# Kernel optimization log

Hardware: AMD Instinct MI355X
Metric: run time of the kernel (lower is better)

## Reference

```python
import jax, jax.numpy as jnp
import numpy as np

B, N, C, H = 8, 4096, 384, 8
HD = C // H  # 48
KERNEL_EPS = 1e-3
EPS = 1e-8


def setup_inputs() -> dict:
    key = jax.random.key(0)
    k1, k2, k3, k4 = jax.random.split(key, 4)
    x = jax.random.normal(k1, (B, N, C), dtype=jnp.float32)
    Wqkv = jax.random.normal(k2, (3 * C, C), dtype=jnp.float32) * 0.02
    Wproj = jax.random.normal(k3, (C, C), dtype=jnp.float32) * 0.02
    bproj = jax.random.normal(k4, (C,), dtype=jnp.float32) * 0.02
    return {"x": x, "Wqkv": Wqkv, "Wproj": Wproj, "bproj": bproj}


def reference(x, Wqkv, Wproj, bproj):
    # qkv projection (no bias): (B,N,3C) -> (3,B,H,N,HD)
    qkv = jnp.einsum('bnc,dc->bnd', x, Wqkv).reshape(B, N, 3, H, HD)
    qkv = jnp.transpose(qkv, (2, 0, 3, 1, 4))
    q, k, v = qkv[0], qkv[1], qkv[2]

    # generalized_kernel with projection_matrix=None, kernel_fn=ReLU
    dn = HD ** (-0.25)  # data normalizer
    qp = jax.nn.relu(dn * q) + KERNEL_EPS  # (B,H,N,HD) feature map, m=HD
    kp = jax.nn.relu(dn * k) + KERNEL_EPS

    ks = kp.sum(axis=2)                              # (B,H,m)
    D = jnp.einsum('bhnm,bhm->bhn', qp, ks)          # (B,H,N)
    kptv = jnp.einsum('bhnd,bhnm->bhdm', v, kp)      # (B,H,HD,m)
    out = jnp.einsum('bhnm,bhdm->bhnd', qp, kptv) / (D[..., None] + EPS)

    # faithful to original: reshape (B,H,N,HD) -> (B,N,C) WITHOUT head transpose
    out = out.reshape(B, N, C)
    return jnp.einsum('bnc,dc->bnd', out, Wproj) + bproj
```

## Files before the change

kernel.cpp:

```cpp
#include <hip/hip_runtime.h>
#include <hip/hip_bf16.h>


typedef __attribute__((ext_vector_type(8))) short short8;
typedef __attribute__((ext_vector_type(4))) float floatx4;

#define MFMA(a, b, c) __builtin_amdgcn_mfma_f32_16x16x32_bf16((a), (b), (c), 0, 0, 0)

__device__ __forceinline__ unsigned short f2bf(float f) {
  union { float f; unsigned u; } x; x.f = f;
  unsigned r = x.u + 0x7FFFu + ((x.u >> 16) & 1u);
  return (unsigned short)(r >> 16);
}

__device__ __forceinline__ void cv4(const float* __restrict__ in, unsigned short* __restrict__ out, int i) {
  float4 v = *(const float4*)(in + i);
  uint2 o;
  o.x = (unsigned)f2bf(v.x) | ((unsigned)f2bf(v.y) << 16);
  o.y = (unsigned)f2bf(v.z) | ((unsigned)f2bf(v.w) << 16);
  *(uint2*)(out + i) = o;
}

__global__ void conv_all(const float* __restrict__ x, const float* __restrict__ wq,
                         const float* __restrict__ wp,
                         unsigned short* __restrict__ xb, unsigned short* __restrict__ wqb,
                         unsigned short* __restrict__ wpb, float* __restrict__ accD) {
  const int tid = blockIdx.x * blockDim.x + threadIdx.x;
  const int stride = gridDim.x * blockDim.x * 4;
  for (int i = tid * 4; i < 12582912; i += stride) cv4(x, xb, i);
  for (int i = tid * 4; i < 442368; i += stride) cv4(wq, wqb, i);
  for (int i = tid * 4; i < 147456; i += stride) cv4(wp, wpb, i);
  float4 z = {0.f, 0.f, 0.f, 0.f};
  for (int i = tid * 4; i < 196608; i += stride) *(float4*)(accD + i) = z;
}

template <int EPI>
__global__ __launch_bounds__(256, 3) void gemm_bt(
    const unsigned short* __restrict__ A,
    const unsigned short* __restrict__ Bt,
    void* __restrict__ Cout,
    unsigned short* __restrict__ Kt,
    unsigned short* __restrict__ Vt,
    const float* __restrict__ bias,
    int M, int N, int K, int ldc) {
  __shared__ unsigned short As[128 * 64];
  __shared__ unsigned short Bs[128 * 64];
  const int NT = N >> 7;
  const int cpx = gridDim.x >> 3;
  const int bid = (blockIdx.x & 7) * cpx + (blockIdx.x >> 3);
  const int bn = bid % NT;
  const int bm = bid / NT;
  const int tid = threadIdx.x;
  const int w = tid >> 6, lane = tid & 63;
  const int wm = w >> 1, wn = w & 1;
  const int l15 = lane & 15, l4 = lane >> 4;

  floatx4 zero = {0.f, 0.f, 0.f, 0.f};
  floatx4 acc[4][4];
#pragma unroll
  for (int i = 0; i < 4; ++i)
#pragma unroll
    for (int j = 0; j < 4; ++j) acc[i][j] = zero;

  const int li0 = (w * 4) * 64 + lane;
  const size_t Abase = (size_t)(bm * 128) * K;
  const size_t Bbase = (size_t)(bn * 128) * K;

  for (int k0 = 0; k0 < K; k0 += 64) {
#pragma unroll
    for (int i = 0; i < 4; ++i) {
      int li = li0 + i * 64;
      int row = li >> 3;
      int col = (li & 7) << 3;
      const unsigned short* gA = A + Abase + (size_t)row * K + k0 + col;
      const unsigned short* gB = Bt + Bbase + (size_t)row * K + k0 + col;
      __builtin_amdgcn_global_load_lds((const __attribute__((address_space(1))) void*)gA,
                                       (__attribute__((address_space(3))) void*)&As[(w * 4 + i) * 512],
                                       16, 0, 0);
      __builtin_amdgcn_global_load_lds((const __attribute__((address_space(1))) void*)gB,
                                       (__attribute__((address_space(3))) void*)&Bs[(w * 4 + i) * 512],
                                       16, 0, 0);
    }
    __syncthreads();
#pragma unroll
    for (int kk = 0; kk < 2; ++kk) {
      short8 a[4], b[4];
#pragma unroll
      for (int mf = 0; mf < 4; ++mf)
        a[mf] = *(const short8*)&As[(wm * 64 + mf * 16 + l15) * 64 + kk * 32 + l4 * 8];
#pragma unroll
      for (int nf = 0; nf < 4; ++nf)
        b[nf] = *(const short8*)&Bs[(wn * 64 + nf * 16 + l15) * 64 + kk * 32 + l4 * 8];
#pragma unroll
      for (int mf = 0; mf < 4; ++mf)
#pragma unroll
        for (int nf = 0; nf < 4; ++nf)
          acc[mf][nf] = MFMA(a[mf], b[nf], acc[mf][nf]);
    }
    __syncthreads();
  }

  const float DN = 0.3799178430f;
  if (EPI == 1) {
#pragma unroll
    for (int mf = 0; mf < 4; ++mf) {
#pragma unroll
      for (int nf = 0; nf < 4; ++nf) {
        int gm0 = bm * 128 + wm * 64 + mf * 16 + l4 * 4;
        int gn = bn * 128 + wn * 64 + nf * 16 + l15;
#pragma unroll
        for (int r = 0; r < 4; ++r)
          ((float*)Cout)[(size_t)(gm0 + r) * ldc + gn] = acc[mf][nf][r] + bias[gn];
      }
    }
  } else if (bn < 3) {
#pragma unroll
    for (int mf = 0; mf < 4; ++mf) {
#pragma unroll
      for (int nf = 0; nf < 4; ++nf) {
        int gm0 = bm * 128 + wm * 64 + mf * 16 + l4 * 4;
        int gn = bn * 128 + wn * 64 + nf * 16 + l15;
#pragma unroll
        for (int r = 0; r < 4; ++r) {
          float v = fmaxf(acc[mf][nf][r] * DN, 0.f) + 1e-3f;
          ((unsigned short*)Cout)[(size_t)(gm0 + r) * 384 + gn] = f2bf(v);
        }
      }
    }
  } else {
    const int isV = (bn >= 6);
    unsigned short* T = isV ? Vt : Kt;
    const int fbase = bn * 128 - (isV ? 768 : 384) + wn * 64;
    const int b = (bm * 128) >> 12;
    const int tokb = ((bm * 128) & 4095) + wm * 64;
#pragma unroll
    for (int nf = 0; nf < 4; ++nf) {
      int fk = fbase + nf * 16 + l15;
      int h = fk / 48;
      int m = fk - h * 48;
      unsigned short* dst = T + (((size_t)(b * 8 + h) * 48 + m) << 12);
#pragma unroll
      for (int mf = 0; mf < 4; ++mf) {
        int tok = tokb + mf * 16 + l4 * 4;
        float v0 = acc[mf][nf][0], v1 = acc[mf][nf][1];
        float v2 = acc[mf][nf][2], v3 = acc[mf][nf][3];
        if (!isV) {
          v0 = fmaxf(v0 * DN, 0.f) + 1e-3f;
          v1 = fmaxf(v1 * DN, 0.f) + 1e-3f;
          v2 = fmaxf(v2 * DN, 0.f) + 1e-3f;
          v3 = fmaxf(v3 * DN, 0.f) + 1e-3f;
        }
        uint2 o;
        o.x = (unsigned)f2bf(v0) | ((unsigned)f2bf(v1) << 16);
        o.y = (unsigned)f2bf(v2) | ((unsigned)f2bf(v3) << 16);
        *(uint2*)(dst + tok) = o;
      }
    }
  }
}

__global__ __launch_bounds__(256, 4) void attn_ksum(
    const unsigned short* __restrict__ Kt,
    const unsigned short* __restrict__ Vt,
    float* __restrict__ accD) {
  const int bh = blockIdx.x >> 3, g = blockIdx.x & 7;
  const int tid = threadIdx.x, w = tid >> 6, lane = tid & 63;
  const int l15 = lane & 15, l4 = lane >> 4;
  __shared__ float red[64 * 48];

  floatx4 zero = {0.f, 0.f, 0.f, 0.f};
  floatx4 acc[4][3];
#pragma unroll
  for (int i = 0; i < 4; ++i)
#pragma unroll
    for (int j = 0; j < 3; ++j) acc[i][j] = zero;

  unsigned short ov = (l15 == 0) ? (unsigned short)0x3F80 : (unsigned short)0;
  short8 ones;
#pragma unroll
  for (int e = 0; e < 8; ++e) ones[e] = (short)ov;

  const size_t base = (size_t)bh * 48 * 4096;
  const int tok0 = g * 512 + w * 128 + l4 * 8;

#pragma unroll
  for (int c = 0; c < 4; ++c) {
    int t0 = tok0 + c * 32;
    short8 a[3], bb[3];
#pragma unroll
    for (int f = 0; f < 3; ++f) {
      a[f] = *(const short8*)&Vt[base + (size_t)(f * 16 + l15) * 4096 + t0];
      bb[f] = *(const short8*)&Kt[base + (size_t)(f * 16 + l15) * 4096 + t0];
    }
#pragma unroll
    for (int af = 0; af < 3; ++af)
#pragma unroll
      for (int bf = 0; bf < 3; ++bf)
        acc[af][bf] = MFMA(a[af], bb[bf], acc[af][bf]);
#pragma unroll
    for (int bf = 0; bf < 3; ++bf)
      acc[3][bf] = MFMA(ones, bb[bf], acc[3][bf]);
  }

  for (int i = tid; i < 64 * 48; i += 256) red[i] = 0.f;
  __syncthreads();
#pragma unroll
  for (int af = 0; af < 4; ++af)
#pragma unroll
    for (int bf = 0; bf < 3; ++bf)
#pragma unroll
      for (int r = 0; r < 4; ++r)
        atomicAdd(&red[(af * 16 + l4 * 4 + r) * 48 + bf * 16 + l15], acc[af][bf][r]);
  __syncthreads();
  float* dst = accD + (size_t)bh * 64 * 48;
  for (int i = tid; i < 64 * 48; i += 256) atomicAdd(&dst[i], red[i]);
}

__global__ __launch_bounds__(256, 2) void attn_out(
    const unsigned short* __restrict__ qp,
    const float* __restrict__ accD,
    unsigned short* __restrict__ outr) {
  const int bh = blockIdx.x >> 4, tg = blockIdx.x & 15;
  const int b = bh >> 3, h = bh & 7;
  const int tid = threadIdx.x, w = tid >> 6, lane = tid & 63;
  const int l15 = lane & 15, l4 = lane >> 4;
  const int t0 = tg * 256 + w * 64;

  short8 bfr[2][4];
#pragma unroll
  for (int kk = 0; kk < 2; ++kk) {
#pragma unroll
    for (int nf = 0; nf < 4; ++nf) {
      int row = nf * 16 + l15;
      int c0 = kk * 32 + l4 * 8;
      short8 f;
      if (kk == 1 && l4 >= 2) {
#pragma unroll
        for (int e = 0; e < 8; ++e) f[e] = 0;
      } else {
        const float* p = accD + (size_t)bh * 3072 + row * 48 + c0;
        float4 v0 = *(const float4*)p;
        float4 v1 = *(const float4*)(p + 4);
        f[0] = (short)f2bf(v0.x); f[1] = (short)f2bf(v0.y);
        f[2] = (short)f2bf(v0.z); f[3] = (short)f2bf(v0.w);
        f[4] = (short)f2bf(v1.x); f[5] = (short)f2bf(v1.y);
        f[6] = (short)f2bf(v1.z); f[7] = (short)f2bf(v1.w);
      }
      bfr[kk][nf] = f;
    }
  }

  floatx4 zero = {0.f, 0.f, 0.f, 0.f};
  floatx4 acc[4][4];
#pragma unroll
  for (int i = 0; i < 4; ++i)
#pragma unroll
    for (int j = 0; j < 4; ++j) acc[i][j] = zero;

  const size_t rb = (size_t)b * 4096;
#pragma unroll
  for (int mf = 0; mf < 4; ++mf) {
#pragma unroll
    for (int kk = 0; kk < 2; ++kk) {
      int tt = t0 + mf * 16 + l15;
      short8 a = *(const short8*)&qp[(rb + tt) * 384 + h * 48 + kk * 32 + l4 * 8];
#pragma unroll
      for (int nf = 0; nf < 4; ++nf)
        acc[mf][nf] = MFMA(a, bfr[kk][nf], acc[mf][nf]);
    }
  }

#pragma unroll
  for (int mf = 0; mf < 4; ++mf) {
    float den[4];
#pragma unroll
    for (int r = 0; r < 4; ++r)
      den[r] = __shfl(acc[mf][3][r], lane & 48, 64) + 1e-8f;
#pragma unroll
    for (int nf = 0; nf < 3; ++nf) {
#pragma unroll
      for (int r = 0; r < 4; ++r) {
        int tt = t0 + mf * 16 + l4 * 4 + r;
        int d = nf * 16 + l15;
        float v = acc[mf][nf][r] / den[r];
        int np = h * 512 + (tt >> 3);
        int cp = (tt & 7) * 48 + d;
        outr[(rb + np) * 384 + cp] = f2bf(v);
      }
    }
  }
}

extern "C" void kernel_launch(void* const* d_in, const int* in_sizes, int n_in,
                              void* d_out, int out_size, void* d_ws, size_t ws_size,
                              hipStream_t stream) {
  const float* x = (const float*)d_in[0];
  const float* Wqkv = (const float*)d_in[1];
  const float* Wproj = (const float*)d_in[2];
  const float* bproj = (const float*)d_in[3];

  char* ws = (char*)d_ws;
  unsigned short* xb = (unsigned short*)(ws);
  unsigned short* wqkvb = (unsigned short*)(ws + 25165824);
  unsigned short* wprojb = (unsigned short*)(ws + 26050560);
  unsigned short* qp = (unsigned short*)(ws + 26345472);
  unsigned short* Kt = (unsigned short*)(ws + 51511552);
  unsigned short* Vt = (unsigned short*)(ws + 76677376);
  float* accD = (float*)(ws + 101843200);
  unsigned short* outr = (unsigned short*)(ws + 102629632);

  conv_all<<<2048, 256, 0, stream>>>(x, Wqkv, Wproj, xb, wqkvb, wprojb, accD);
  gemm_bt<0><<<2304, 256, 0, stream>>>(xb, wqkvb, (void*)qp, Kt, Vt, nullptr, 32768, 1152, 384, 384);
  attn_ksum<<<512, 256, 0, stream>>>(Kt, Vt, accD);
  attn_out<<<1024, 256, 0, stream>>>(qp, accD, outr);
  gemm_bt<1><<<768, 256, 0, stream>>>(outr, wprojb, d_out, nullptr, nullptr, bproj, 32768, 384, 384, 384);
}
```

Before: 224.0 us.

## Fuse x conversion and K^T V reduction into the QKV GEMM

The QKV GEMM now reads fp32 x directly and converts it to bf16 while staging into shared memory, which removes the separate full-size x conversion pass. K and V tiles for each head are kept in shared memory and reduced immediately into the K^T V and K-sum accumulators with MFMA and global atomics. This drops the Kt/Vt intermediate buffers and the attn_ksum kernel. In exchange the GEMM loads A with non-async vector loads, uses more shared memory (fewer blocks per CU), launches more blocks, and issues many more global atomics.

```diff
diff --git a/kernel.cpp b/kernel.cpp
--- a/kernel.cpp
+++ b/kernel.cpp
@@ -21,199 +21,169 @@
   *(uint2*)(out + i) = o;
 }
 
-__global__ void conv_all(const float* __restrict__ x, const float* __restrict__ wq,
-                         const float* __restrict__ wp,
-                         unsigned short* __restrict__ xb, unsigned short* __restrict__ wqb,
-                         unsigned short* __restrict__ wpb, float* __restrict__ accD) {
+__global__ void conv_w(const float* __restrict__ wq, const float* __restrict__ wp,
+                       unsigned short* __restrict__ wqb, unsigned short* __restrict__ wpb,
+                       float* __restrict__ accD) {
   const int tid = blockIdx.x * blockDim.x + threadIdx.x;
   const int stride = gridDim.x * blockDim.x * 4;
-  for (int i = tid * 4; i < 12582912; i += stride) cv4(x, xb, i);
   for (int i = tid * 4; i < 442368; i += stride) cv4(wq, wqb, i);
   for (int i = tid * 4; i < 147456; i += stride) cv4(wp, wpb, i);
   float4 z = {0.f, 0.f, 0.f, 0.f};
   for (int i = tid * 4; i < 196608; i += stride) *(float4*)(accD + i) = z;
 }
 
-template <int EPI>
-__global__ __launch_bounds__(256, 3) void gemm_bt(
-    const unsigned short* __restrict__ A,
-    const unsigned short* __restrict__ Bt,
-    void* __restrict__ Cout,
-    unsigned short* __restrict__ Kt,
-    unsigned short* __restrict__ Vt,
-    const float* __restrict__ bias,
-    int M, int N, int K, int ldc) {
+__global__ __launch_bounds__(256, 2) void gemm_qkv(
+    const float* __restrict__ x,
+    const unsigned short* __restrict__ Wq,
+    unsigned short* __restrict__ qp,
+    float* __restrict__ accD) {
   __shared__ unsigned short As[128 * 64];
   __shared__ unsigned short Bs[128 * 64];
-  const int NT = N >> 7;
+  __shared__ unsigned short Tt[2][48 * 136];
+
   const int cpx = gridDim.x >> 3;
   const int bid = (blockIdx.x & 7) * cpx + (blockIdx.x >> 3);
-  const int bn = bid % NT;
-  const int bm = bid / NT;
+  const int mt = bid / 11;
+  const int j = bid - mt * 11;
   const int tid = threadIdx.x;
   const int w = tid >> 6, lane = tid & 63;
   const int wm = w >> 1, wn = w & 1;
   const int l15 = lane & 15, l4 = lane >> 4;
+  const int isQ = (j < 3);
+  const int h = j - 3;
 
   floatx4 zero = {0.f, 0.f, 0.f, 0.f};
   floatx4 acc[4][4];
 #pragma unroll
   for (int i = 0; i < 4; ++i)
 #pragma unroll
-    for (int j = 0; j < 4; ++j) acc[i][j] = zero;
-
-  const int li0 = (w * 4) * 64 + lane;
-  const size_t Abase = (size_t)(bm * 128) * K;
-  const size_t Bbase = (size_t)(bn * 128) * K;
-
-  for (int k0 = 0; k0 < K; k0 += 64) {
-#pragma unroll
-    for (int i = 0; i < 4; ++i) {
-      int li = li0 + i * 64;
-      int row = li >> 3;
-      int col = (li & 7) << 3;
-      const unsigned short* gA = A + Abase + (size_t)row * K + k0 + col;
-      const unsigned short* gB = Bt + Bbase + (size_t)row * K + k0 + col;
-      __builtin_amdgcn_global_load_lds((const __attribute__((address_space(1))) void*)gA,
-                                       (__attribute__((address_space(3))) void*)&As[(w * 4 + i) * 512],
-                                       16, 0, 0);
-      __builtin_amdgcn_global_load_lds((const __attribute__((address_space(1))) void*)gB,
-                                       (__attribute__((address_space(3))) void*)&Bs[(w * 4 + i) * 512],
-                                       16, 0, 0);
+    for (int jj = 0; jj < 4; ++jj) acc[i][jj] = zero;
+
+  const size_t Abase = (size_t)mt * 128 * 384;
+  const int arow = tid >> 4;
+  const int akf = (tid & 15) * 4;
+
+  for (int k0 = 0; k0 < 384; k0 += 64) {
+#pragma unroll
+    for (int p = 0; p < 8; ++p) {
+      int row = p * 16 + arow;
+      float4 v = *(const float4*)&x[Abase + (size_t)row * 384 + k0 + akf];
+      uint2 o;
+      o.x = (unsigned)f2bf(v.x) | ((unsigned)f2bf(v.y) << 16);
+      o.y = (unsigned)f2bf(v.z) | ((unsigned)f2bf(v.w) << 16);
+      *(uint2*)&As[row * 64 + akf] = o;
+    }
+    if (isQ) {
+      const size_t Bb = (size_t)(j * 128) * 384;
+#pragma unroll
+      for (int i = 0; i < 4; ++i) {
+        int li = w * 256 + i * 64 + lane;
+        int row = li >> 3, col = (li & 7) << 3;
+        __builtin_amdgcn_global_load_lds(
+            (const __attribute__((address_space(1))) void*)(Wq + Bb + (size_t)row * 384 + k0 + col),
+            (__attribute__((address_space(3))) void*)&Bs[row * 64 + col], 16, 0, 0);
+      }
+    } else {
+#pragma unroll
+      for (int i = 0; i < 3; ++i) {
+        int idx = i * 256 + tid;
+        int row = idx >> 3, col = (idx & 7) << 3;
+        int srow = (row < 48) ? (384 + h * 48 + row) : (720 + h * 48 + row);
+        __builtin_amdgcn_global_load_lds(
+            (const __attribute__((address_space(1))) void*)(Wq + (size_t)srow * 384 + k0 + col),
+            (__attribute__((address_space(3))) void*)&Bs[row * 64 + col], 16, 0, 0);
+      }
     }
     __syncthreads();
 #pragma unroll
     for (int kk = 0; kk < 2; ++kk) {
-      short8 a[4], b[4];
+      short8 a[4];
 #pragma unroll
       for (int mf = 0; mf < 4; ++mf)
         a[mf] = *(const short8*)&As[(wm * 64 + mf * 16 + l15) * 64 + kk * 32 + l4 * 8];
-#pragma unroll
-      for (int nf = 0; nf < 4; ++nf)
-        b[nf] = *(const short8*)&Bs[(wn * 64 + nf * 16 + l15) * 64 + kk * 32 + l4 * 8];
-#pragma unroll
-      for (int mf = 0; mf < 4; ++mf)
-#pragma unroll
-        for (int nf = 0; nf < 4; ++nf)
-          acc[mf][nf] = MFMA(a[mf], b[nf], acc[mf][nf]);
+      if (isQ) {
+#pragma unroll
+        for (int nf = 0; nf < 4; ++nf) {
+          short8 b = *(const short8*)&Bs[(wn * 64 + nf * 16 + l15) * 64 + kk * 32 + l4 * 8];
+#pragma unroll
+          for (int mf = 0; mf < 4; ++mf) acc[mf][nf] = MFMA(a[mf], b, acc[mf][nf]);
+        }
+      } else {
+#pragma unroll
+        for (int nf = 0; nf < 3; ++nf) {
+          short8 b = *(const short8*)&Bs[(wn * 48 + nf * 16 + l15) * 64 + kk * 32 + l4 * 8];
+#pragma unroll
+          for (int mf = 0; mf < 4; ++mf) acc[mf][nf] = MFMA(a[mf], b, acc[mf][nf]);
+        }
+      }
     }
     __syncthreads();
   }
 
   const float DN = 0.3799178430f;
-  if (EPI == 1) {
+  if (isQ) {
 #pragma unroll
     for (int mf = 0; mf < 4; ++mf) {
 #pragma unroll
       for (int nf = 0; nf < 4; ++nf) {
-        int gm0 = bm * 128 + wm * 64 + mf * 16 + l4 * 4;
-        int gn = bn * 128 + wn * 64 + nf * 16 + l15;
-#pragma unroll
-        for (int r = 0; r < 4; ++r)
-          ((float*)Cout)[(size_t)(gm0 + r) * ldc + gn] = acc[mf][nf][r] + bias[gn];
-      }
-    }
-  } else if (bn < 3) {
-#pragma unroll
-    for (int mf = 0; mf < 4; ++mf) {
-#pragma unroll
-      for (int nf = 0; nf < 4; ++nf) {
-        int gm0 = bm * 128 + wm * 64 + mf * 16 + l4 * 4;
-        int gn = bn * 128 + wn * 64 + nf * 16 + l15;
+        int gm0 = mt * 128 + wm * 64 + mf * 16 + l4 * 4;
+        int gn = j * 128 + wn * 64 + nf * 16 + l15;
 #pragma unroll
         for (int r = 0; r < 4; ++r) {
           float v = fmaxf(acc[mf][nf][r] * DN, 0.f) + 1e-3f;
-          ((unsigned short*)Cout)[(size_t)(gm0 + r) * 384 + gn] = f2bf(v);
+          qp[(size_t)(gm0 + r) * 384 + gn] = f2bf(v);
         }
       }
     }
   } else {
-    const int isV = (bn >= 6);
-    unsigned short* T = isV ? Vt : Kt;
-    const int fbase = bn * 128 - (isV ? 768 : 384) + wn * 64;
-    const int b = (bm * 128) >> 12;
-    const int tokb = ((bm * 128) & 4095) + wm * 64;
-#pragma unroll
-    for (int nf = 0; nf < 4; ++nf) {
-      int fk = fbase + nf * 16 + l15;
-      int h = fk / 48;
-      int m = fk - h * 48;
-      unsigned short* dst = T + (((size_t)(b * 8 + h) * 48 + m) << 12);
+#pragma unroll
+    for (int nf = 0; nf < 3; ++nf) {
 #pragma unroll
       for (int mf = 0; mf < 4; ++mf) {
-        int tok = tokb + mf * 16 + l4 * 4;
-        float v0 = acc[mf][nf][0], v1 = acc[mf][nf][1];
-        float v2 = acc[mf][nf][2], v3 = acc[mf][nf][3];
-        if (!isV) {
-          v0 = fmaxf(v0 * DN, 0.f) + 1e-3f;
-          v1 = fmaxf(v1 * DN, 0.f) + 1e-3f;
-          v2 = fmaxf(v2 * DN, 0.f) + 1e-3f;
-          v3 = fmaxf(v3 * DN, 0.f) + 1e-3f;
+#pragma unroll
+        for (int r = 0; r < 4; ++r) {
+          float v = acc[mf][nf][r];
+          if (wn == 0) v = fmaxf(v * DN, 0.f) + 1e-3f;
+          Tt[wn][(nf * 16 + l15) * 136 + wm * 64 + mf * 16 + l4 * 4 + r] = f2bf(v);
         }
-        uint2 o;
-        o.x = (unsigned)f2bf(v0) | ((unsigned)f2bf(v1) << 16);
-        o.y = (unsigned)f2bf(v2) | ((unsigned)f2bf(v3) << 16);
-        *(uint2*)(dst + tok) = o;
-      }
-    }
-  }
-}
-
-__global__ __launch_bounds__(256, 4) void attn_ksum(
-    const unsigned short* __restrict__ Kt,
-    const unsigned short* __restrict__ Vt,
-    float* __restrict__ accD) {
-  const int bh = blockIdx.x >> 3, g = blockIdx.x & 7;
-  const int tid = threadIdx.x, w = tid >> 6, lane = tid & 63;
-  const int l15 = lane & 15, l4 = lane >> 4;
-  __shared__ float red[64 * 48];
-
-  floatx4 zero = {0.f, 0.f, 0.f, 0.f};
-  floatx4 acc[4][3];
-#pragma unroll
-  for (int i = 0; i < 4; ++i)
-#pragma unroll
-    for (int j = 0; j < 3; ++j) acc[i][j] = zero;
-
-  unsigned short ov = (l15 == 0) ? (unsigned short)0x3F80 : (unsigned short)0;
-  short8 ones;
-#pragma unroll
-  for (int e = 0; e < 8; ++e) ones[e] = (short)ov;
-
-  const size_t base = (size_t)bh * 48 * 4096;
-  const int tok0 = g * 512 + w * 128 + l4 * 8;
-
-#pragma unroll
-  for (int c = 0; c < 4; ++c) {
-    int t0 = tok0 + c * 32;
-    short8 a[3], bb[3];
-#pragma unroll
-    for (int f = 0; f < 3; ++f) {
-      a[f] = *(const short8*)&Vt[base + (size_t)(f * 16 + l15) * 4096 + t0];
-      bb[f] = *(const short8*)&Kt[base + (size_t)(f * 16 + l15) * 4096 + t0];
-    }
-#pragma unroll
-    for (int af = 0; af < 3; ++af)
-#pragma unroll
-      for (int bf = 0; bf < 3; ++bf)
-        acc[af][bf] = MFMA(a[af], bb[bf], acc[af][bf]);
-#pragma unroll
-    for (int bf = 0; bf < 3; ++bf)
-      acc[3][bf] = MFMA(ones, bb[bf], acc[3][bf]);
-  }
-
-  for (int i = tid; i < 64 * 48; i += 256) red[i] = 0.f;
-  __syncthreads();
-#pragma unroll
-  for (int af = 0; af < 4; ++af)
-#pragma unroll
-    for (int bf = 0; bf < 3; ++bf)
-#pragma unroll
-      for (int r = 0; r < 4; ++r)
-        atomicAdd(&red[(af * 16 + l4 * 4 + r) * 48 + bf * 16 + l15], acc[af][bf][r]);
-  __syncthreads();
-  float* dst = accD + (size_t)bh * 64 * 48;
-  for (int i = tid; i < 64 * 48; i += 256) atomicAdd(&dst[i], red[i]);
+      }
+    }
+    __syncthreads();
+    short8 ones;
+    {
+      unsigned short ov = (l15 == 0) ? (unsigned short)0x3F80 : (unsigned short)0;
+#pragma unroll
+      for (int e = 0; e < 8; ++e) ones[e] = (short)ov;
+    }
+    floatx4 acc2[3];
+#pragma unroll
+    for (int i = 0; i < 3; ++i) acc2[i] = zero;
+#pragma unroll
+    for (int c = 0; c < 4; ++c) {
+      short8 af;
+      if (w < 3)
+        af = *(const short8*)&Tt[1][(w * 16 + l15) * 136 + c * 32 + l4 * 8];
+      else
+        af = ones;
+#pragma unroll
+      for (int mfr = 0; mfr < 3; ++mfr) {
+        short8 bf8 = *(const short8*)&Tt[0][(mfr * 16 + l15) * 136 + c * 32 + l4 * 8];
+        acc2[mfr] = MFMA(af, bf8, acc2[mfr]);
+      }
+    }
+    float* dst = accD + (size_t)((mt >> 5) * 8 + h) * 3072;
+    if (w < 3) {
+#pragma unroll
+      for (int mfr = 0; mfr < 3; ++mfr)
+#pragma unroll
+        for (int r = 0; r < 4; ++r)
+          atomicAdd(&dst[(w * 16 + l4 * 4 + r) * 48 + mfr * 16 + l15], acc2[mfr][r]);
+    } else if (l4 == 0) {
+#pragma unroll
+      for (int mfr = 0; mfr < 3; ++mfr)
+        atomicAdd(&dst[48 * 48 + mfr * 16 + l15], acc2[mfr][0]);
+    }
+  }
 }
 
 __global__ __launch_bounds__(256, 2) void attn_out(
@@ -291,6 +261,79 @@
   }
 }
 
+__global__ __launch_bounds__(256, 2) void gemm_proj(
+    const unsigned short* __restrict__ A,
+    const unsigned short* __restrict__ Bt,
+    float* __restrict__ Cout,
+    const float* __restrict__ bias) {
+  __shared__ unsigned short As[128 * 64];
+  __shared__ unsigned short Bs[128 * 64];
+  const int NT = 3;
+  const int cpx = gridDim.x >> 3;
+  const int bid = (blockIdx.x & 7) * cpx + (blockIdx.x >> 3);
+  const int bn = bid % NT;
+  const int bm = bid / NT;
+  const int tid = threadIdx.x;
+  const int w = tid >> 6, lane = tid & 63;
+  const int wm = w >> 1, wn = w & 1;
+  const int l15 = lane & 15, l4 = lane >> 4;
+
+  floatx4 zero = {0.f, 0.f, 0.f, 0.f};
+  floatx4 acc[4][4];
+#pragma unroll
+  for (int i = 0; i < 4; ++i)
+#pragma unroll
+    for (int j = 0; j < 4; ++j) acc[i][j] = zero;
+
+  const int li0 = (w * 4) * 64 + lane;
+  const size_t Abase = (size_t)(bm * 128) * 384;
+  const size_t Bbase = (size_t)(bn * 128) * 384;
+
+  for (int k0 = 0; k0 < 384; k0 += 64) {
+#pragma unroll
+    for (int i = 0; i < 4; ++i) {
+      int li = li0 + i * 64;
+      int row = li >> 3;
+      int col = (li & 7) << 3;
+      __builtin_amdgcn_global_load_lds(
+          (const __attribute__((address_space(1))) void*)(A + Abase + (size_t)row * 384 + k0 + col),
+          (__attribute__((address_space(3))) void*)&As[(w * 4 + i) * 512], 16, 0, 0);
+      __builtin_amdgcn_global_load_lds(
+          (const __attribute__((address_space(1))) void*)(Bt + Bbase + (size_t)row * 384 + k0 + col),
+          (__attribute__((address_space(3))) void*)&Bs[(w * 4 + i) * 512], 16, 0, 0);
+    }
+    __syncthreads();
+#pragma unroll
+    for (int kk = 0; kk < 2; ++kk) {
+      short8 a[4], b[4];
+#pragma unroll
+      for (int mf = 0; mf < 4; ++mf)
+        a[mf] = *(const short8*)&As[(wm * 64 + mf * 16 + l15) * 64 + kk * 32 + l4 * 8];
+#pragma unroll
+      for (int nf = 0; nf < 4; ++nf)
+        b[nf] = *(const short8*)&Bs[(wn * 64 + nf * 16 + l15) * 64 + kk * 32 + l4 * 8];
+#pragma unroll
+      for (int mf = 0; mf < 4; ++mf)
+#pragma unroll
+        for (int nf = 0; nf < 4; ++nf)
+          acc[mf][nf] = MFMA(a[mf], b[nf], acc[mf][nf]);
+    }
+    __syncthreads();
+  }
+
+#pragma unroll
+  for (int mf = 0; mf < 4; ++mf) {
+#pragma unroll
+    for (int nf = 0; nf < 4; ++nf) {
+      int gm0 = bm * 128 + wm * 64 + mf * 16 + l4 * 4;
+      int gn = bn * 128 + wn * 64 + nf * 16 + l15;
+#pragma unroll
+      for (int r = 0; r < 4; ++r)
+        Cout[(size_t)(gm0 + r) * 384 + gn] = acc[mf][nf][r] + bias[gn];
+    }
+  }
+}
+
 extern "C" void kernel_launch(void* const* d_in, const int* in_sizes, int n_in,
                               void* d_out, int out_size, void* d_ws, size_t ws_size,
                               hipStream_t stream) {
@@ -300,18 +343,14 @@
   const float* bproj = (const float*)d_in[3];
 
   char* ws = (char*)d_ws;
-  unsigned short* xb = (unsigned short*)(ws);
-  unsigned short* wqkvb = (unsigned short*)(ws + 25165824);
-  unsigned short* wprojb = (unsigned short*)(ws + 26050560);
-  unsigned short* qp = (unsigned short*)(ws + 26345472);
-  unsigned short* Kt = (unsigned short*)(ws + 51511552);
-  unsigned short* Vt = (unsigned short*)(ws + 76677376);
-  float* accD = (float*)(ws + 101843200);
-  unsigned short* outr = (unsigned short*)(ws + 102629632);
-
-  conv_all<<<2048, 256, 0, stream>>>(x, Wqkv, Wproj, xb, wqkvb, wprojb, accD);
-  gemm_bt<0><<<2304, 256, 0, stream>>>(xb, wqkvb, (void*)qp, Kt, Vt, nullptr, 32768, 1152, 384, 384);
-  attn_ksum<<<512, 256, 0, stream>>>(Kt, Vt, accD);
+  unsigned short* qp = (unsigned short*)(ws);
+  float* accD = (float*)(ws + 25165824);
+  unsigned short* outr = (unsigned short*)(ws + 25952256);
+  unsigned short* wqkvb = (unsigned short*)(ws + 51118080);
+  unsigned short* wprojb = (unsigned short*)(ws + 52002816);
+
+  conv_w<<<256, 256, 0, stream>>>(Wqkv, Wproj, wqkvb, wprojb, accD);
+  gemm_qkv<<<2816, 256, 0, stream>>>(x, wqkvb, qp, accD);
   attn_out<<<1024, 256, 0, stream>>>(qp, accD, outr);
-  gemm_bt<1><<<768, 256, 0, stream>>>(outr, wprojb, d_out, nullptr, nullptr, bproj, 32768, 384, 384, 384);
-}
+  gemm_proj<<<768, 256, 0, stream>>>(outr, wprojb, (float*)d_out, bproj);
+}
```

After: 207.4 us. -7.4%, faster.
